# Performance work log

Measured on AMD Instinct MI355X. Metric: run time of the kernel, lower is better.

Reference implementation:

```python
import jax, jax.numpy as jnp
import numpy as np

D_MODEL = 1024
N_HEADS = 16
POINT_DIM = 4
PLUCKER_DIM = 6
PAIRS4 = [(0, 1), (0, 2), (0, 3), (1, 2), (1, 3), (2, 3)]
_J6 = jnp.array([[0, 0, 0, 0, 0, 1], [0, 0, 0, 0, -1, 0], [0, 0, 0, 1, 0, 0],
                 [0, 0, 1, 0, 0, 0], [0, -1, 0, 0, 0, 0], [1, 0, 0, 0, 0, 0]], dtype=jnp.float32)


def exterior(p1, p2):
    # p1, p2: [..., point_dim] -> normalized Plucker coords [..., 6]
    L = jnp.stack([p1[..., i] * p2[..., j] - p1[..., j] * p2[..., i] for i, j in PAIRS4], axis=-1)
    n = jnp.linalg.norm(L, axis=-1, keepdims=True)
    return L / jnp.maximum(n, 1e-12)


def setup_inputs() -> dict:
    key = jax.random.key(0)
    ks = jax.random.split(key, 16)
    B, T, D, H, pd = 2, 1024, D_MODEL, N_HEADS, POINT_DIM
    s = 0.02
    return {
        "x": jax.random.normal(ks[0], (B, T, D), dtype=jnp.float32),
        "qkv_w": jax.random.normal(ks[1], (D, 3 * D), dtype=jnp.float32) * s,
        "qkv_b": jnp.zeros((3 * D,), dtype=jnp.float32),
        "w1_write_w": jax.random.normal(ks[2], (2 * D, pd * H), dtype=jnp.float32) * s,
        "w2_write_w": jax.random.normal(ks[3], (D, pd * H), dtype=jnp.float32) * s,
        "w1_read_w": jax.random.normal(ks[4], (D, pd * H), dtype=jnp.float32) * s,
        "w2_read_w": jax.random.normal(ks[5], (D, pd * H), dtype=jnp.float32) * s,
        "mem_value_w": jax.random.normal(ks[6], (D, D), dtype=jnp.float32) * s,
        "mem_value_b": jnp.zeros((D,), dtype=jnp.float32),
        "mem_gate_w": jax.random.normal(ks[7], (D, H), dtype=jnp.float32) * s,
        "mem_gate_b": jnp.zeros((H,), dtype=jnp.float32),
        "mem_scale": jnp.full((H,), 0.1, dtype=jnp.float32),
        "out_w": jax.random.normal(ks[8], (D, D), dtype=jnp.float32) * s,
        "out_b": jnp.zeros((D,), dtype=jnp.float32),
        "decay_logits": jnp.full((H,), 4.6, dtype=jnp.float32),
        "J": _J6,
    }


def reference(x, qkv_w, qkv_b, w1_write_w, w2_write_w, w1_read_w, w2_read_w,
              mem_value_w, mem_value_b, mem_gate_w, mem_gate_b, mem_scale,
              out_w, out_b, decay_logits, J):
    B, T, D = x.shape
    H = N_HEADS
    dh = D // H
    pd = POINT_DIM
    scale = dh ** (-0.5)

    # ---- standard causal attention ----
    qkv = (x @ qkv_w + qkv_b).reshape(B, T, 3, H, dh)
    q = jnp.transpose(qkv[:, :, 0], (0, 2, 1, 3))  # [B,H,T,dh]
    k = jnp.transpose(qkv[:, :, 1], (0, 2, 1, 3))
    v = jnp.transpose(qkv[:, :, 2], (0, 2, 1, 3))
    scores = jnp.einsum('bhtd,bhsd->bhts', q, k) * scale
    causal_mask = jnp.triu(jnp.ones((T, T), dtype=bool), k=1)
    scores = jnp.where(causal_mask, -jnp.inf, scores)
    attn = jax.nn.softmax(scores, axis=-1)
    seq_out = jnp.einsum('bhts,bhsd->bthd', attn, v).reshape(B, T, D)

    # ---- trigram write lines ----
    z = jnp.zeros((B, 1, D), dtype=x.dtype)
    x_prev1 = jnp.concatenate([z, x[:, :-1]], axis=1)
    x_prev2 = jnp.concatenate([z, z, x[:, :-2]], axis=1)
    trigram_ctx = jnp.concatenate([x_prev2, x_prev1], axis=-1)  # [B,T,2D]
    w1 = (trigram_ctx @ w1_write_w).reshape(B, T, H, pd)
    w2 = (x @ w2_write_w).reshape(B, T, H, pd)
    write_lines = exterior(w1, w2)  # [B,T,H,6]
    r1 = (x @ w1_read_w).reshape(B, T, H, pd)
    r2 = (x @ w2_read_w).reshape(B, T, H, pd)
    read_lines = exterior(r1, r2)  # [B,T,H,6]

    # ---- Plucker incidence + decay weighting ----
    J_write = jnp.einsum('bshi,ij->bshj', write_lines, J)
    incidence = jnp.einsum('bthi,bshi->bhts', read_lines, J_write)  # [B,H,T,T]
    incidence_sq = incidence ** 2
    positions = jnp.arange(T, dtype=x.dtype)
    diffs = positions[:, None] - positions[None, :]  # [T,T]
    decays = jax.nn.sigmoid(decay_logits)  # [H]
    # strictly-causal (diffs>0) decay weights; masked_fill(triu diag=0, 0) == (diffs>0)
    weights = jnp.where(diffs[None] > 0, decays[:, None, None] ** jnp.maximum(diffs, 0.0)[None], 0.0)
    mem_score = jnp.sum(incidence_sq * weights[None], axis=-1)  # [B,H,T]

    # ---- gated memory value ----
    mem_val = x @ mem_value_w + mem_value_b  # [B,T,D]
    gate = jax.nn.sigmoid(x @ mem_gate_w + mem_gate_b)  # [B,T,H]
    mem_score_t = jnp.transpose(mem_score, (0, 2, 1))  # [B,T,H]
    gated = jax.nn.sigmoid(mem_score_t * mem_scale[None, None, :]) * gate
    gated = jnp.mean(gated, axis=-1, keepdims=True)  # [B,T,1]

    return (seq_out + gated * mem_val) @ out_w + out_b
```

## Files before the change

kernel.cpp:

```cpp
#include <hip/hip_runtime.h>
#include <hip/hip_bf16.h>
#include <stdint.h>


typedef __attribute__((ext_vector_type(8))) __bf16 bf16v8;
typedef __attribute__((ext_vector_type(8))) short  s16x8;
typedef __attribute__((ext_vector_type(4))) float  f32x4;

#define LOG2E 1.4426950408889634f

__device__ __forceinline__ float bf2f(short s) {
  union { uint32_t u; float f; } cv; cv.u = ((uint32_t)(uint16_t)s) << 16; return cv.f;
}
__device__ __forceinline__ short f2bf(float f) {
  union { float f; uint32_t u; } cv; cv.f = f;
  uint32_t r = cv.u + 0x7fffu + ((cv.u >> 16) & 1u);
  return (short)(r >> 16);
}

__device__ __forceinline__ f32x4 mfma_bf16(s16x8 a, s16x8 b, f32x4 c) {
  return __builtin_amdgcn_mfma_f32_16x16x32_bf16(
      __builtin_bit_cast(bf16v8, a), __builtin_bit_cast(bf16v8, b), c, 0, 0, 0);
}

__device__ __forceinline__ void gload_lds16(const void* g, void* l) {
  __builtin_amdgcn_global_load_lds(
      (const __attribute__((address_space(1))) uint32_t*)g,
      (__attribute__((address_space(3))) uint32_t*)l, 16, 0, 0);
}


__global__ __launch_bounds__(256) void k_prep(
    const float* __restrict__ x, const float* __restrict__ qkvw,
    const float* __restrict__ mvw, const float* __restrict__ ow,
    const float* __restrict__ w1w, const float* __restrict__ w2w,
    const float* __restrict__ r1w, const float* __restrict__ r2w,
    const float* __restrict__ gw, const float* __restrict__ qkvb,
    const float* __restrict__ mvb,
    short* __restrict__ xb, short* __restrict__ btall, short* __restrict__ owT,
    float* __restrict__ biasAll) {
  __shared__ float tile[32][33];
  const int bid = blockIdx.x;
  const int tid = threadIdx.x;
  if (bid < 2048) {
    const int i = (bid * 256 + tid) * 4;
    float4 v = *(const float4*)&x[i];
    short4 o;
    o.x = f2bf(v.x); o.y = f2bf(v.y); o.z = f2bf(v.z); o.w = f2bf(v.w);
    *(short4*)&xb[i] = o;
    return;
  }
  if (bid < 7168) {
    const float* W; short* Wt; int N, u;
    if (bid < 5120)      { W = qkvw; Wt = btall;                       N = 3072; u = bid - 2048; }
    else if (bid < 6144) { W = mvw;  Wt = btall + (size_t)3072 * 1024; N = 1024; u = bid - 5120; }
    else                 { W = ow;   Wt = owT;                         N = 1024; u = bid - 6144; }
    const int ntiles = N >> 5;
    const int n0 = (u % ntiles) * 32, k0 = (u / ntiles) * 32;
    const int tx = tid & 31, ty = tid >> 5;
#pragma unroll
    for (int i = 0; i < 4; i++)
      tile[ty + i * 8][tx] = W[(size_t)(k0 + ty + i * 8) * N + n0 + tx];
    __syncthreads();
#pragma unroll
    for (int i = 0; i < 4; i++)
      Wt[(size_t)(n0 + ty + i * 8) * 1024 + k0 + tx] = f2bf(tile[tx][ty + i * 8]);
    return;
  }
  if (bid < 8704) {
    const int idx = (bid - 7168) * 256 + tid;
    const int r = idx >> 10, k = idx & 1023;
    float v = 0.f;
    if (r < 64)       v = w1w[(size_t)k * 64 + r];
    else if (r < 128) v = w1w[(size_t)(1024 + k) * 64 + (r - 64)];
    else if (r < 192) v = w2w[(size_t)k * 64 + (r - 128)];
    else if (r < 256) v = r1w[(size_t)k * 64 + (r - 192)];
    else if (r < 320) v = r2w[(size_t)k * 64 + (r - 256)];
    else if (r < 336) v = gw[(size_t)k * 16 + (r - 320)];
    btall[(size_t)4096 * 1024 + idx] = f2bf(v);
    return;
  }
  {
    const int i = (bid - 8704) * 256 + tid;
    if (i < 4480) {
      float v = 0.f;
      if (i < 3072) v = qkvb[i];
      else if (i < 4096) v = mvb[i - 3072];
      biasAll[i] = v;
    }
  }
}


__global__ __launch_bounds__(256) void k_gemmF(const short* __restrict__ A,
                                               const short* __restrict__ Bt,
                                               short* __restrict__ C,
                                               const float* __restrict__ bias,
                                               float* __restrict__ projf) {
  const int N = 4480, K = 1024;
  __shared__ short As[2][128 * 32];
  __shared__ short Bs[2][128 * 32];
  const int m0 = blockIdx.x * 128, n0 = blockIdx.y * 128;
  const int tid = threadIdx.x;
  const int lane = tid & 63, w = tid >> 6;
  const int wr = (w >> 1) * 64, wc = (w & 1) * 64;
  const int l15 = lane & 15, lg = lane >> 4;
  const int r0e = tid >> 2, c0e = (tid & 3) << 3;
  const int r1e = (tid + 256) >> 2, c1e = ((tid + 256) & 3) << 3;
  f32x4 acc[4][4] = {};

  gload_lds16(A + (size_t)(m0 + r0e) * K + c0e, &As[0][tid * 8]);
  gload_lds16(A + (size_t)(m0 + r1e) * K + c1e, &As[0][(tid + 256) * 8]);
  gload_lds16(Bt + (size_t)(n0 + r0e) * K + c0e, &Bs[0][tid * 8]);
  gload_lds16(Bt + (size_t)(n0 + r1e) * K + c1e, &Bs[0][(tid + 256) * 8]);
  __syncthreads();

  const int nkt = K >> 5;
  for (int kt = 0; kt < nkt; kt++) {
    const int cur = kt & 1;
    if (kt + 1 < nkt) {
      const int k0n = (kt + 1) << 5;
      const int nxt = cur ^ 1;
      gload_lds16(A + (size_t)(m0 + r0e) * K + k0n + c0e, &As[nxt][tid * 8]);
      gload_lds16(A + (size_t)(m0 + r1e) * K + k0n + c1e, &As[nxt][(tid + 256) * 8]);
      gload_lds16(Bt + (size_t)(n0 + r0e) * K + k0n + c0e, &Bs[nxt][tid * 8]);
      gload_lds16(Bt + (size_t)(n0 + r1e) * K + k0n + c1e, &Bs[nxt][(tid + 256) * 8]);
    }
    s16x8 af[4], bfv[4];
#pragma unroll
    for (int i = 0; i < 4; i++) {
      af[i]  = *(const s16x8*)&As[cur][(wr + i * 16 + l15) * 32 + lg * 8];
      bfv[i] = *(const s16x8*)&Bs[cur][(wc + i * 16 + l15) * 32 + lg * 8];
    }
    __builtin_amdgcn_s_setprio(1);
#pragma unroll
    for (int mi = 0; mi < 4; mi++)
#pragma unroll
      for (int ni = 0; ni < 4; ni++)
        acc[mi][ni] = mfma_bf16(af[mi], bfv[ni], acc[mi][ni]);
    __builtin_amdgcn_s_setprio(0);
    __syncthreads();
  }
  const bool isproj = (n0 >= 4096);
#pragma unroll
  for (int mi = 0; mi < 4; mi++)
#pragma unroll
    for (int ni = 0; ni < 4; ni++) {
      const int col = n0 + wc + ni * 16 + l15;
      const float bv = bias[col];
#pragma unroll
      for (int r = 0; r < 4; r++) {
        const int row = m0 + wr + mi * 16 + lg * 4 + r;
        const float v = acc[mi][ni][r] + bv;
        if (isproj) projf[(size_t)row * 384 + (col - 4096)] = v;
        else        C[(size_t)row * 4480 + col] = f2bf(v);
      }
    }
}


template <int BM>
__global__ __launch_bounds__(256) void k_gemm(const short* __restrict__ A,
                                              const short* __restrict__ Bt,
                                              float* __restrict__ C,
                                              const float* __restrict__ bias,
                                              int N, int K) {
  constexpr int MI = BM / 32;
  __shared__ short As[2][BM * 32];
  __shared__ short Bs[2][128 * 32];
  const int m0 = blockIdx.x * BM, n0 = blockIdx.y * 128;
  const int tid = threadIdx.x;
  const int lane = tid & 63, w = tid >> 6;
  const int wr = (w >> 1) * (BM / 2), wc = (w & 1) * 64;
  const int l15 = lane & 15, lg = lane >> 4;
  const int r0e = tid >> 2, c0e = (tid & 3) << 3;
  const int r1e = (tid + 256) >> 2, c1e = ((tid + 256) & 3) << 3;
  f32x4 acc[MI][4] = {};

  auto stage = [&](int buf, int k0) {
    if constexpr (BM == 128) {
      gload_lds16(A + (size_t)(m0 + r0e) * K + k0 + c0e, &As[buf][tid * 8]);
      gload_lds16(A + (size_t)(m0 + r1e) * K + k0 + c1e, &As[buf][(tid + 256) * 8]);
    } else {
      gload_lds16(A + (size_t)(m0 + r0e) * K + k0 + c0e, &As[buf][tid * 8]);
    }
    gload_lds16(Bt + (size_t)(n0 + r0e) * K + k0 + c0e, &Bs[buf][tid * 8]);
    gload_lds16(Bt + (size_t)(n0 + r1e) * K + k0 + c1e, &Bs[buf][(tid + 256) * 8]);
  };

  stage(0, 0);
  __syncthreads();
  const int nkt = K >> 5;
  for (int kt = 0; kt < nkt; kt++) {
    const int cur = kt & 1;
    if (kt + 1 < nkt) stage(cur ^ 1, (kt + 1) << 5);
    s16x8 af[MI], bfv[4];
#pragma unroll
    for (int i = 0; i < MI; i++)
      af[i] = *(const s16x8*)&As[cur][(wr + i * 16 + l15) * 32 + lg * 8];
#pragma unroll
    for (int i = 0; i < 4; i++)
      bfv[i] = *(const s16x8*)&Bs[cur][(wc + i * 16 + l15) * 32 + lg * 8];
    __builtin_amdgcn_s_setprio(1);
#pragma unroll
    for (int mi = 0; mi < MI; mi++)
#pragma unroll
      for (int ni = 0; ni < 4; ni++)
        acc[mi][ni] = mfma_bf16(af[mi], bfv[ni], acc[mi][ni]);
    __builtin_amdgcn_s_setprio(0);
    __syncthreads();
  }
#pragma unroll
  for (int mi = 0; mi < MI; mi++)
#pragma unroll
    for (int ni = 0; ni < 4; ni++) {
      const int col = n0 + wc + ni * 16 + l15;
      const float bv = bias ? bias[col] : 0.f;
#pragma unroll
      for (int r = 0; r < 4; r++) {
        const int row = m0 + wr + mi * 16 + lg * 4 + r;
        C[(size_t)row * N + col] = acc[mi][ni][r] + bv;
      }
    }
}


__global__ void k_vtr(const short* __restrict__ fused, short* __restrict__ vtg) {
  __shared__ short tile[32][33];
  const int bh = blockIdx.z;
  const int b = bh >> 4, h = bh & 15;
  const int t0 = blockIdx.x * 32, d0 = blockIdx.y * 32;
  const int tx = threadIdx.x, ty = threadIdx.y;
#pragma unroll
  for (int i = 0; i < 4; i++)
    tile[ty + i * 8][tx] =
        fused[(size_t)(b * 1024 + t0 + ty + i * 8) * 4480 + 2048 + h * 64 + d0 + tx];
  __syncthreads();
#pragma unroll
  for (int i = 0; i < 4; i++)
    vtg[(size_t)(bh * 64 + d0 + ty + i * 8) * 1024 + t0 + tx] = tile[tx][ty + i * 8];
}


__global__ __launch_bounds__(256) void k_attn(const short* __restrict__ fused,
                                              const short* __restrict__ vtg,
                                              float* __restrict__ Of,
                                              float* __restrict__ Ml) {
  const int id = blockIdx.x;
  const int j = 15 - (id >> 6);
  const int rem = id & 63;
  const int sid = rem >> 5, bh = rem & 31;
  const int b = bh >> 4, h = bh & 15;
  const int tid = threadIdx.x, lane = tid & 63, w = tid >> 6;
  const int l15 = lane & 15, lg = lane >> 4;
  const int q0 = j * 64;
  const int nkv = j + 1;
  const int half = (nkv + 1) >> 1;
  const int lo = sid ? half : 0;
  const int hi = sid ? nkv : half;
  const int pidx = ((j * 32 + bh) << 1) | sid;

  __shared__ short Kl[64 * 72];
  __shared__ short Vt[64 * 72];
  __shared__ short Pl[4][16 * 72];
  const short* base = fused + (size_t)b * 1024 * 4480;
  const short* vbase = vtg + (size_t)bh * 64 * 1024;

  const int e0 = tid, e1 = tid + 256;
  const int r0e = e0 >> 3, c0e = (e0 & 7) << 3;
  const int r1e = e1 >> 3, c1e = (e1 & 7) << 3;

  s16x8 qf[2];
#pragma unroll
  for (int ks = 0; ks < 2; ks++)
    qf[ks] = *(const s16x8*)&base[(size_t)(q0 + w * 16 + l15) * 4480 +
                                  h * 64 + ks * 32 + lg * 8];

  f32x4 O[4] = {};
  float m_run[4], l_run[4];
#pragma unroll
  for (int r = 0; r < 4; r++) { m_run[r] = -1e30f; l_run[r] = 0.f; }

  if (lo < hi) {
    const int kv0 = lo * 64;
    s16x8 ka = *(const s16x8*)&base[(size_t)(kv0 + r0e) * 4480 + 1024 + h * 64 + c0e];
    s16x8 kb = *(const s16x8*)&base[(size_t)(kv0 + r1e) * 4480 + 1024 + h * 64 + c1e];
    s16x8 va = *(const s16x8*)&vbase[(size_t)r0e * 1024 + kv0 + c0e];
    s16x8 vb = *(const s16x8*)&vbase[(size_t)r1e * 1024 + kv0 + c1e];
    *(s16x8*)&Kl[r0e * 72 + c0e] = ka;
    *(s16x8*)&Kl[r1e * 72 + c1e] = kb;
    *(s16x8*)&Vt[r0e * 72 + c0e] = va;
    *(s16x8*)&Vt[r1e * 72 + c1e] = vb;
  }
  __syncthreads();

  for (int kt = lo; kt < hi; kt++) {
    const int kv0 = kt * 64;
    const bool pf = (kt + 1 < hi);
    s16x8 kn0, kn1, vn0, vn1;
    if (pf) {
      const int kvn = kv0 + 64;
      kn0 = *(const s16x8*)&base[(size_t)(kvn + r0e) * 4480 + 1024 + h * 64 + c0e];
      kn1 = *(const s16x8*)&base[(size_t)(kvn + r1e) * 4480 + 1024 + h * 64 + c1e];
      vn0 = *(const s16x8*)&vbase[(size_t)r0e * 1024 + kvn + c0e];
      vn1 = *(const s16x8*)&vbase[(size_t)r1e * 1024 + kvn + c1e];
    }

    f32x4 S[4] = {};
    __builtin_amdgcn_s_setprio(1);
#pragma unroll
    for (int sf = 0; sf < 4; sf++) {
      s16x8 kf0 = *(const s16x8*)&Kl[(sf * 16 + l15) * 72 + lg * 8];
      s16x8 kf1 = *(const s16x8*)&Kl[(sf * 16 + l15) * 72 + 32 + lg * 8];
      S[sf] = mfma_bf16(qf[0], kf0, S[sf]);
      S[sf] = mfma_bf16(qf[1], kf1, S[sf]);
    }
    __builtin_amdgcn_s_setprio(0);

    const bool diag = (kt == j);
    float sv[4][4];
#pragma unroll
    for (int sf = 0; sf < 4; sf++)
#pragma unroll
      for (int r = 0; r < 4; r++) {
        float vv = S[sf][r] * 0.125f;
        if (diag) {
          const int sg = kv0 + sf * 16 + l15;
          const int qg = q0 + w * 16 + lg * 4 + r;
          if (sg > qg) vv = -1e30f;
        }
        sv[sf][r] = vv;
      }
#pragma unroll
    for (int r = 0; r < 4; r++) {
      float pm = fmaxf(fmaxf(sv[0][r], sv[1][r]), fmaxf(sv[2][r], sv[3][r]));
      pm = fmaxf(pm, __shfl_xor(pm, 1, 64));
      pm = fmaxf(pm, __shfl_xor(pm, 2, 64));
      pm = fmaxf(pm, __shfl_xor(pm, 4, 64));
      pm = fmaxf(pm, __shfl_xor(pm, 8, 64));
      if (pm > m_run[r] + 8.f) {
        const float fac = exp2f((m_run[r] - pm) * LOG2E);
        m_run[r] = pm;
        l_run[r] *= fac;
#pragma unroll
        for (int nf = 0; nf < 4; nf++) O[nf][r] *= fac;
      }
      float rs = 0.f;
#pragma unroll
      for (int sf = 0; sf < 4; sf++) {
        float p = (sv[sf][r] <= -1e29f) ? 0.f : exp2f((sv[sf][r] - m_run[r]) * LOG2E);
        rs += p;
        Pl[w][(lg * 4 + r) * 72 + sf * 16 + l15] = f2bf(p);
      }
      rs += __shfl_xor(rs, 1, 64);
      rs += __shfl_xor(rs, 2, 64);
      rs += __shfl_xor(rs, 4, 64);
      rs += __shfl_xor(rs, 8, 64);
      l_run[r] += rs;
    }

    __builtin_amdgcn_s_setprio(1);
#pragma unroll
    for (int ks = 0; ks < 2; ks++) {
      s16x8 pfr = *(const s16x8*)&Pl[w][l15 * 72 + ks * 32 + lg * 8];
#pragma unroll
      for (int nf = 0; nf < 4; nf++) {
        s16x8 vf = *(const s16x8*)&Vt[(nf * 16 + l15) * 72 + ks * 32 + lg * 8];
        O[nf] = mfma_bf16(pfr, vf, O[nf]);
      }
    }
    __builtin_amdgcn_s_setprio(0);

    __syncthreads();
    if (pf) {
      *(s16x8*)&Kl[r0e * 72 + c0e] = kn0;
      *(s16x8*)&Kl[r1e * 72 + c1e] = kn1;
      *(s16x8*)&Vt[r0e * 72 + c0e] = vn0;
      *(s16x8*)&Vt[r1e * 72 + c1e] = vn1;
      __syncthreads();
    }
  }

  float* ob = Of + (size_t)pidx * 4096;
  float* mb = Ml + (size_t)pidx * 128;
#pragma unroll
  for (int r = 0; r < 4; r++) {
    const int rloc = w * 16 + lg * 4 + r;
#pragma unroll
    for (int nf = 0; nf < 4; nf++)
      ob[rloc * 64 + nf * 16 + l15] = O[nf][r];
    if (l15 == 0) {
      mb[rloc] = m_run[r];
      mb[64 + rloc] = l_run[r];
    }
  }
}


__device__ __forceinline__ void exterior6(const float p1[4], const float p2[4], float L[6]) {
  L[0] = p1[0] * p2[1] - p1[1] * p2[0];
  L[1] = p1[0] * p2[2] - p1[2] * p2[0];
  L[2] = p1[0] * p2[3] - p1[3] * p2[0];
  L[3] = p1[1] * p2[2] - p1[2] * p2[1];
  L[4] = p1[1] * p2[3] - p1[3] * p2[1];
  L[5] = p1[2] * p2[3] - p1[3] * p2[2];
  float n = sqrtf(L[0] * L[0] + L[1] * L[1] + L[2] * L[2] +
                  L[3] * L[3] + L[4] * L[4] + L[5] * L[5]);
  float inv = 1.f / fmaxf(n, 1e-12f);
#pragma unroll
  for (int j = 0; j < 6; j++) L[j] *= inv;
}


__global__ __launch_bounds__(1024) void k_mscan(const float* __restrict__ proj,
                                                const float* __restrict__ Jm,
                                                const float* __restrict__ dlog,
                                                float* __restrict__ ms) {
  const int bh = blockIdx.x;
  const int b = bh >> 4, h = bh & 15;
  const int t = threadIdx.x;
  const int lane = t & 63, wv = t >> 6;
  const int n = b * 1024 + t;
  const float d = 1.f / (1.f + expf(-dlog[h]));
  const float l2d = log2f(d);

  float p1[4], p2[4], L[6], Jw[6], rl[6];
#pragma unroll
  for (int p = 0; p < 4; p++) {
    float a  = (t >= 2) ? proj[(size_t)(n - 2) * 384 + h * 4 + p] : 0.f;
    float bb = (t >= 1) ? proj[(size_t)(n - 1) * 384 + 64 + h * 4 + p] : 0.f;
    p1[p] = a + bb;
    p2[p] = proj[(size_t)n * 384 + 128 + h * 4 + p];
  }
  exterior6(p1, p2, L);
#pragma unroll
  for (int j = 0; j < 6; j++) {
    float s = 0.f;
#pragma unroll
    for (int i = 0; i < 6; i++) s += L[i] * Jm[i * 6 + j];
    Jw[j] = s;
  }
#pragma unroll
  for (int p = 0; p < 4; p++) {
    p1[p] = proj[(size_t)n * 384 + 192 + h * 4 + p];
    p2[p] = proj[(size_t)n * 384 + 256 + h * 4 + p];
  }
  exterior6(p1, p2, rl);

  const float ws = exp2f(-(float)t * l2d);
  float c[21], loc[21];
  {
    int k = 0;
#pragma unroll
    for (int i = 0; i < 6; i++)
#pragma unroll
      for (int j = i; j < 6; j++) {
        loc[k] = ws * Jw[i] * Jw[j];
        c[k] = loc[k];
        k++;
      }
  }
#pragma unroll
  for (int off = 1; off < 64; off <<= 1) {
#pragma unroll
    for (int k = 0; k < 21; k++) {
      float u = __shfl_up(c[k], off, 64);
      if (lane >= off) c[k] += u;
    }
  }
  __shared__ float wsum[16][21];
  __shared__ float woff[16][21];
  if (lane == 63)
#pragma unroll
    for (int k = 0; k < 21; k++) wsum[wv][k] = c[k];
  __syncthreads();
  if (t < 21) {
    float run = 0.f;
    for (int w2 = 0; w2 < 16; w2++) { woff[w2][t] = run; run += wsum[w2][t]; }
  }
  __syncthreads();
  float q = 0.f;
  {
    int k = 0;
#pragma unroll
    for (int i = 0; i < 6; i++)
#pragma unroll
      for (int j = i; j < 6; j++) {
        const float P = woff[wv][k] + (c[k] - loc[k]);
        q += (i == j ? 1.f : 2.f) * rl[i] * rl[j] * P;
        k++;
      }
  }
  ms[(size_t)n * 16 + h] = exp2f((float)t * l2d) * q;
}


__global__ __launch_bounds__(256) void k_combine(const float* __restrict__ Of,
                                                 const float* __restrict__ Ml,
                                                 const short* __restrict__ fused,
                                                 const float* __restrict__ proj,
                                                 const float* __restrict__ ms,
                                                 const float* __restrict__ mem_scale,
                                                 const float* __restrict__ gate_b,
                                                 short* __restrict__ comb) {
  const int n = blockIdx.x;
  const int tid = threadIdx.x;
  __shared__ float gsh;
  if (tid < 16) {
    const float gp = proj[(size_t)n * 384 + 320 + tid] + gate_b[tid];
    const float g = 1.f / (1.f + expf(-gp));
    const float sc = ms[(size_t)n * 16 + tid] * mem_scale[tid];
    const float sg = 1.f / (1.f + expf(-sc));
    float v = sg * g;
    v += __shfl_xor(v, 1, 64);
    v += __shfl_xor(v, 2, 64);
    v += __shfl_xor(v, 4, 64);
    v += __shfl_xor(v, 8, 64);
    if (tid == 0) gsh = v * (1.f / 16.f);
  }
  __syncthreads();
  const float g = gsh;
  const int b = n >> 10, t = n & 1023;
  const int c0 = tid * 4;
  const int h = c0 >> 6, coff = c0 & 63;
  const int bh = b * 16 + h;
  const int p = ((t >> 6) * 32 + bh) << 1;
  const int rloc = t & 63;
  const float m0v = Ml[(size_t)p * 128 + rloc];
  const float l0v = Ml[(size_t)p * 128 + 64 + rloc];
  const float m1v = Ml[(size_t)(p + 1) * 128 + rloc];
  const float l1v = Ml[(size_t)(p + 1) * 128 + 64 + rloc];
  const float M = fmaxf(m0v, m1v);
  const float w0 = exp2f((m0v - M) * LOG2E);
  const float w1 = exp2f((m1v - M) * LOG2E);
  const float inv = 1.f / (w0 * l0v + w1 * l1v);
  f32x4 o0 = *(const f32x4*)&Of[(size_t)p * 4096 + rloc * 64 + coff];
  f32x4 o1 = *(const f32x4*)&Of[(size_t)(p + 1) * 4096 + rloc * 64 + coff];
  short4 mvv = *(const short4*)&fused[(size_t)n * 4480 + 3072 + c0];
  short4 ov;
  ov.x = f2bf((w0 * o0[0] + w1 * o1[0]) * inv + g * bf2f(mvv.x));
  ov.y = f2bf((w0 * o0[1] + w1 * o1[1]) * inv + g * bf2f(mvv.y));
  ov.z = f2bf((w0 * o0[2] + w1 * o1[2]) * inv + g * bf2f(mvv.z));
  ov.w = f2bf((w0 * o0[3] + w1 * o1[3]) * inv + g * bf2f(mvv.w));
  *(short4*)&comb[(size_t)n * 1024 + c0] = ov;
}


extern "C" void kernel_launch(void* const* d_in, const int* in_sizes, int n_in,
                              void* d_out, int out_size, void* d_ws, size_t ws_size,
                              hipStream_t stream) {
  const float* x    = (const float*)d_in[0];
  const float* qkvw = (const float*)d_in[1];
  const float* qkvb = (const float*)d_in[2];
  const float* w1w  = (const float*)d_in[3];
  const float* w2w  = (const float*)d_in[4];
  const float* r1w  = (const float*)d_in[5];
  const float* r2w  = (const float*)d_in[6];
  const float* mvw  = (const float*)d_in[7];
  const float* mvb  = (const float*)d_in[8];
  const float* gw   = (const float*)d_in[9];
  const float* gb   = (const float*)d_in[10];
  const float* msc  = (const float*)d_in[11];
  const float* ow   = (const float*)d_in[12];
  const float* ob   = (const float*)d_in[13];
  const float* dlog = (const float*)d_in[14];
  const float* Jm   = (const float*)d_in[15];
  float* out = (float*)d_out;

  char* wsp = (char*)d_ws;
  auto alloc = [&](size_t bytes) {
    char* p = wsp;
    wsp += (bytes + 255) & ~(size_t)255;
    return p;
  };
  short* xb     = (short*)alloc((size_t)2048 * 1024 * 2);
  short* btall  = (short*)alloc((size_t)4480 * 1024 * 2);
  short* owT    = (short*)alloc((size_t)1024 * 1024 * 2);
  short* fusedC = (short*)alloc((size_t)2048 * 4480 * 2);
  float* projf  = (float*)alloc((size_t)2048 * 384 * 4);
  float* biasA  = (float*)alloc((size_t)4480 * 4);
  short* vtg    = (short*)alloc((size_t)32 * 64 * 1024 * 2);
  short* comb   = (short*)alloc((size_t)2048 * 1024 * 2);
  float* msb    = (float*)alloc((size_t)2048 * 16 * 4);
  float* Of     = (float*)alloc((size_t)1024 * 4096 * 4);
  float* Mlb    = (float*)alloc((size_t)1024 * 128 * 4);

  k_prep<<<8722, 256, 0, stream>>>(x, qkvw, mvw, ow, w1w, w2w, r1w, r2w, gw,
                                   qkvb, mvb, xb, btall, owT, biasA);

  k_gemmF<<<dim3(16, 35), 256, 0, stream>>>(xb, btall, fusedC, biasA, projf);

  k_vtr<<<dim3(32, 2, 32), dim3(32, 8), 0, stream>>>(fusedC, vtg);
  k_attn<<<1024, 256, 0, stream>>>(fusedC, vtg, Of, Mlb);

  k_mscan<<<32, 1024, 0, stream>>>(projf, Jm, dlog, msb);
  k_combine<<<2048, 256, 0, stream>>>(Of, Mlb, fusedC, projf, msb, msc, gb, comb);

  k_gemm<64><<<dim3(32, 8), 256, 0, stream>>>(comb, owT, out, ob, 1024, 1024);
}
```

Measured before the change: 117.3 us.

## Deepen GEMM LDS pipeline to four stages and fuse V transpose into GEMM epilogue

```diff
diff --git a/kernel.cpp b/kernel.cpp
--- a/kernel.cpp
+++ b/kernel.cpp
@@ -96,10 +96,12 @@
                                                const short* __restrict__ Bt,
                                                short* __restrict__ C,
                                                const float* __restrict__ bias,
-                                               float* __restrict__ projf) {
+                                               float* __restrict__ projf,
+                                               short* __restrict__ vtg) {
   const int N = 4480, K = 1024;
-  __shared__ short As[2][128 * 32];
-  __shared__ short Bs[2][128 * 32];
+  __shared__ short pool[32768];
+  short* Asp = pool;
+  short* Bsp = pool + 16384;
   const int m0 = blockIdx.x * 128, n0 = blockIdx.y * 128;
   const int tid = threadIdx.x;
   const int lane = tid & 63, w = tid >> 6;
@@ -109,39 +111,68 @@
   const int r1e = (tid + 256) >> 2, c1e = ((tid + 256) & 3) << 3;
   f32x4 acc[4][4] = {};
 
-  gload_lds16(A + (size_t)(m0 + r0e) * K + c0e, &As[0][tid * 8]);
-  gload_lds16(A + (size_t)(m0 + r1e) * K + c1e, &As[0][(tid + 256) * 8]);
-  gload_lds16(Bt + (size_t)(n0 + r0e) * K + c0e, &Bs[0][tid * 8]);
-  gload_lds16(Bt + (size_t)(n0 + r1e) * K + c1e, &Bs[0][(tid + 256) * 8]);
+  auto stage = [&](int buf, int k0) {
+    gload_lds16(A + (size_t)(m0 + r0e) * K + k0 + c0e, Asp + buf * 4096 + tid * 8);
+    gload_lds16(A + (size_t)(m0 + r1e) * K + k0 + c1e, Asp + buf * 4096 + (tid + 256) * 8);
+    gload_lds16(Bt + (size_t)(n0 + r0e) * K + k0 + c0e, Bsp + buf * 4096 + tid * 8);
+    gload_lds16(Bt + (size_t)(n0 + r1e) * K + k0 + c1e, Bsp + buf * 4096 + (tid + 256) * 8);
+  };
+
+  stage(0, 0);
+  stage(1, 32);
   __syncthreads();
 
   const int nkt = K >> 5;
-  for (int kt = 0; kt < nkt; kt++) {
-    const int cur = kt & 1;
-    if (kt + 1 < nkt) {
-      const int k0n = (kt + 1) << 5;
-      const int nxt = cur ^ 1;
-      gload_lds16(A + (size_t)(m0 + r0e) * K + k0n + c0e, &As[nxt][tid * 8]);
-      gload_lds16(A + (size_t)(m0 + r1e) * K + k0n + c1e, &As[nxt][(tid + 256) * 8]);
-      gload_lds16(Bt + (size_t)(n0 + r0e) * K + k0n + c0e, &Bs[nxt][tid * 8]);
-      gload_lds16(Bt + (size_t)(n0 + r1e) * K + k0n + c1e, &Bs[nxt][(tid + 256) * 8]);
-    }
-    s16x8 af[4], bfv[4];
-#pragma unroll
-    for (int i = 0; i < 4; i++) {
-      af[i]  = *(const s16x8*)&As[cur][(wr + i * 16 + l15) * 32 + lg * 8];
-      bfv[i] = *(const s16x8*)&Bs[cur][(wc + i * 16 + l15) * 32 + lg * 8];
-    }
-    __builtin_amdgcn_s_setprio(1);
+  for (int kp = 0; kp < nkt; kp += 2) {
+    if (kp + 2 < nkt) stage((kp + 2) & 3, (kp + 2) << 5);
+    if (kp + 3 < nkt) stage((kp + 3) & 3, (kp + 3) << 5);
+#pragma unroll
+    for (int u = 0; u < 2; u++) {
+      const int cur = (kp + u) & 3;
+      s16x8 af[4], bfv[4];
+#pragma unroll
+      for (int i = 0; i < 4; i++) {
+        af[i]  = *(const s16x8*)&Asp[cur * 4096 + (wr + i * 16 + l15) * 32 + lg * 8];
+        bfv[i] = *(const s16x8*)&Bsp[cur * 4096 + (wc + i * 16 + l15) * 32 + lg * 8];
+      }
+      __builtin_amdgcn_s_setprio(1);
+#pragma unroll
+      for (int mi = 0; mi < 4; mi++)
+#pragma unroll
+        for (int ni = 0; ni < 4; ni++)
+          acc[mi][ni] = mfma_bf16(af[mi], bfv[ni], acc[mi][ni]);
+      __builtin_amdgcn_s_setprio(0);
+    }
+    __syncthreads();
+  }
+
+  const bool isproj = (n0 >= 4096);
+  const bool isv = (n0 >= 2048) && (n0 < 3072);
+  if (isv) {
+    short* T = pool;
 #pragma unroll
     for (int mi = 0; mi < 4; mi++)
 #pragma unroll
-      for (int ni = 0; ni < 4; ni++)
-        acc[mi][ni] = mfma_bf16(af[mi], bfv[ni], acc[mi][ni]);
-    __builtin_amdgcn_s_setprio(0);
+      for (int ni = 0; ni < 4; ni++) {
+        const int colLoc = wc + ni * 16 + l15;
+        const float bv = bias[n0 + colLoc];
+#pragma unroll
+        for (int r = 0; r < 4; r++)
+          T[colLoc * 136 + wr + mi * 16 + lg * 4 + r] = f2bf(acc[mi][ni][r] + bv);
+      }
     __syncthreads();
-  }
-  const bool isproj = (n0 >= 4096);
+    const int b = m0 >> 10, t0 = m0 & 1023;
+#pragma unroll
+    for (int q = 0; q < 8; q++) {
+      const int colLoc = w * 32 + q * 4 + (lane >> 4);
+      const int chunk = lane & 15;
+      s16x8 v = *(const s16x8*)&T[colLoc * 136 + chunk * 8];
+      const int cd = n0 + colLoc - 2048;
+      const int hh = cd >> 6, d = cd & 63;
+      *(s16x8*)&vtg[((size_t)((b << 4) + hh) * 64 + d) * 1024 + t0 + chunk * 8] = v;
+    }
+    return;
+  }
 #pragma unroll
   for (int mi = 0; mi < 4; mi++)
 #pragma unroll
@@ -166,8 +197,8 @@
                                               const float* __restrict__ bias,
                                               int N, int K) {
   constexpr int MI = BM / 32;
-  __shared__ short As[2][BM * 32];
-  __shared__ short Bs[2][128 * 32];
+  __shared__ short As[4][BM * 32];
+  __shared__ short Bs[4][128 * 32];
   const int m0 = blockIdx.x * BM, n0 = blockIdx.y * 128;
   const int tid = threadIdx.x;
   const int lane = tid & 63, w = tid >> 6;
@@ -189,25 +220,30 @@
   };
 
   stage(0, 0);
+  stage(1, 32);
   __syncthreads();
   const int nkt = K >> 5;
-  for (int kt = 0; kt < nkt; kt++) {
-    const int cur = kt & 1;
-    if (kt + 1 < nkt) stage(cur ^ 1, (kt + 1) << 5);
-    s16x8 af[MI], bfv[4];
-#pragma unroll
-    for (int i = 0; i < MI; i++)
-      af[i] = *(const s16x8*)&As[cur][(wr + i * 16 + l15) * 32 + lg * 8];
-#pragma unroll
-    for (int i = 0; i < 4; i++)
-      bfv[i] = *(const s16x8*)&Bs[cur][(wc + i * 16 + l15) * 32 + lg * 8];
-    __builtin_amdgcn_s_setprio(1);
-#pragma unroll
-    for (int mi = 0; mi < MI; mi++)
-#pragma unroll
-      for (int ni = 0; ni < 4; ni++)
-        acc[mi][ni] = mfma_bf16(af[mi], bfv[ni], acc[mi][ni]);
-    __builtin_amdgcn_s_setprio(0);
+  for (int kp = 0; kp < nkt; kp += 2) {
+    if (kp + 2 < nkt) stage((kp + 2) & 3, (kp + 2) << 5);
+    if (kp + 3 < nkt) stage((kp + 3) & 3, (kp + 3) << 5);
+#pragma unroll
+    for (int u = 0; u < 2; u++) {
+      const int cur = (kp + u) & 3;
+      s16x8 af[MI], bfv[4];
+#pragma unroll
+      for (int i = 0; i < MI; i++)
+        af[i] = *(const s16x8*)&As[cur][(wr + i * 16 + l15) * 32 + lg * 8];
+#pragma unroll
+      for (int i = 0; i < 4; i++)
+        bfv[i] = *(const s16x8*)&Bs[cur][(wc + i * 16 + l15) * 32 + lg * 8];
+      __builtin_amdgcn_s_setprio(1);
+#pragma unroll
+      for (int mi = 0; mi < MI; mi++)
+#pragma unroll
+        for (int ni = 0; ni < 4; ni++)
+          acc[mi][ni] = mfma_bf16(af[mi], bfv[ni], acc[mi][ni]);
+      __builtin_amdgcn_s_setprio(0);
+    }
     __syncthreads();
   }
 #pragma unroll
@@ -222,23 +258,6 @@
         C[(size_t)row * N + col] = acc[mi][ni][r] + bv;
       }
     }
-}
-
-
-__global__ void k_vtr(const short* __restrict__ fused, short* __restrict__ vtg) {
-  __shared__ short tile[32][33];
-  const int bh = blockIdx.z;
-  const int b = bh >> 4, h = bh & 15;
-  const int t0 = blockIdx.x * 32, d0 = blockIdx.y * 32;
-  const int tx = threadIdx.x, ty = threadIdx.y;
-#pragma unroll
-  for (int i = 0; i < 4; i++)
-    tile[ty + i * 8][tx] =
-        fused[(size_t)(b * 1024 + t0 + ty + i * 8) * 4480 + 2048 + h * 64 + d0 + tx];
-  __syncthreads();
-#pragma unroll
-  for (int i = 0; i < 4; i++)
-    vtg[(size_t)(bh * 64 + d0 + ty + i * 8) * 1024 + t0 + tx] = tile[tx][ty + i * 8];
 }
 
 
@@ -588,9 +607,8 @@
   k_prep<<<8722, 256, 0, stream>>>(x, qkvw, mvw, ow, w1w, w2w, r1w, r2w, gw,
                                    qkvb, mvb, xb, btall, owT, biasA);
 
-  k_gemmF<<<dim3(16, 35), 256, 0, stream>>>(xb, btall, fusedC, biasA, projf);
-
-  k_vtr<<<dim3(32, 2, 32), dim3(32, 8), 0, stream>>>(fusedC, vtg);
+  k_gemmF<<<dim3(16, 35), 256, 0, stream>>>(xb, btall, fusedC, biasA, projf, vtg);
+
   k_attn<<<1024, 256, 0, stream>>>(fusedC, vtg, Of, Mlb);
 
   k_mscan<<<32, 1024, 0, stream>>>(projf, Jm, dlog, msb);
```

Result: no change. 116.4 us (median of 3 runs) (-0.8%).
